# Optimization experiments

Measured on AMD Instinct MI355X. Metric: run time of the kernel, lower is better.

The kernel has to match this reference:

```python
import jax, jax.numpy as jnp
import numpy as np

D = 1024          # hidden_dim
S = 128           # seq_len
DECAY = 0.99
SPARSITY = 0.05
INHIB = 1.5       # inhibition_factor
TOPK = max(1, int(D * SPARSITY))  # = 51


def sparsify(x):
    """ReLU + keep top-k fraction (threshold = k-th largest of relu(x))."""
    pos = jax.nn.relu(x)
    thr = jax.lax.top_k(pos, TOPK)[0][-1]  # k-th largest value
    mask = (pos >= thr).astype(pos.dtype)
    return pos * mask


def setup_inputs() -> dict:
    key = jax.random.key(0)
    k1, k2 = jax.random.split(key)
    embeddings = jax.random.normal(k1, (S, D), dtype=jnp.float32)
    contradiction_scores = jax.random.uniform(k2, (S,), dtype=jnp.float32)
    return {"embeddings": embeddings, "contradiction_scores": contradiction_scores}


def reference(embeddings, contradiction_scores):
    """BDHScanner.process_sequence: sequential Hebbian updates with key=value=token.

    Returns (drift_scores [S], states [S, D, D]) — per-token drift and the
    state snapshot after each step, matching the torch module's outputs.
    """
    def step(state, inp):
        x, c = inp
        s = sparsify(x)                      # key == value vector (sparsified once)
        expectation = s @ state              # [D] GEVM against DxD state
        drift = jnp.linalg.norm(s - expectation)
        # excitatory - inhibitory = outer(k, v) * (1 - c * INHIB)
        update = jnp.outer(s, s) * (1.0 - c * INHIB)
        new_state = jax.nn.relu(state * DECAY + update)
        return new_state, (drift, new_state)

    state0 = jnp.zeros((D, D), dtype=jnp.float32)
    _, (drifts, states) = jax.lax.scan(step, state0, (embeddings, contradiction_scores))
    return drifts, states
```

## Files before the change

### kernel.cpp

```cpp
#include <hip/hip_runtime.h>

#define SEQ 128
#define DIM 1024
#define TOPK 51
#define DECAY 0.99f
#define INHIB 1.5f

__global__ __launch_bounds__(256) void sparsify_kernel(
    const float* __restrict__ emb, float* __restrict__ s_out,
    int* __restrict__ nnz_idx, int* __restrict__ nnz_cnt)
{
    const int t   = blockIdx.x;
    const int tid = threadIdx.x;
    const float* x = emb + t * DIM;

    float    v[4];
    unsigned u[4];
#pragma unroll
    for (int e = 0; e < 4; ++e) {
        float val = fmaxf(x[e * 256 + tid], 0.0f);
        v[e] = val;
        u[e] = __float_as_uint(val);
    }

    __shared__ unsigned hist[256];
    __shared__ unsigned sh_prefix;
    __shared__ unsigned sh_k;
    __shared__ int      sh_cnt;
    if (tid == 0) { sh_prefix = 0u; sh_k = TOPK; sh_cnt = 0; }
    __syncthreads();

    for (int pass = 0; pass < 4; ++pass) {
        const int shift = 24 - 8 * pass;
        const unsigned prefix = sh_prefix;
        hist[tid] = 0u;
        __syncthreads();
#pragma unroll
        for (int e = 0; e < 4; ++e) {
            bool ok;
            if (pass == 0) ok = true;
            else           ok = ((u[e] >> (shift + 8)) == (prefix >> (shift + 8)));
            if (ok) atomicAdd(&hist[(u[e] >> shift) & 255u], 1u);
        }
        __syncthreads();
        if (tid == 0) {
            unsigned k = sh_k, cum = 0;
            int b = 255;
            for (; b > 0; --b) { cum += hist[b]; if (cum >= k) break; }
            if (cum < k) { cum += hist[0]; }
            sh_k      = k - (cum - hist[b]);
            sh_prefix = prefix | ((unsigned)b << shift);
        }
        __syncthreads();
    }

    const float thr = __uint_as_float(sh_prefix);
#pragma unroll
    for (int e = 0; e < 4; ++e) {
        const int idx = e * 256 + tid;
        const float sval = (v[e] >= thr) ? v[e] : 0.0f;
        s_out[t * DIM + idx] = sval;
        if (sval > 0.0f) {
            int pos = atomicAdd(&sh_cnt, 1);
            nnz_idx[t * DIM + pos] = idx;
        }
    }
    __syncthreads();
    if (tid == 0) nnz_cnt[t] = sh_cnt;
}

__global__ __launch_bounds__(256) void evolve_kernel(
    const float* __restrict__ s, const float* __restrict__ con,
    float* __restrict__ states)
{
    const int i0 = blockIdx.x * 4;
    const int j0 = threadIdx.x * 4;

    float st[4][4];
#pragma unroll
    for (int a = 0; a < 4; ++a)
#pragma unroll
        for (int b = 0; b < 4; ++b) st[a][b] = 0.0f;

    for (int t = 0; t < SEQ; ++t) {
        const float f = 1.0f - INHIB * con[t];
        const float4 sj = *(const float4*)(s + t * DIM + j0);
        float si[4];
#pragma unroll
        for (int a = 0; a < 4; ++a) si[a] = s[t * DIM + i0 + a] * f;

        float* outp = states + (size_t)t * DIM * DIM;
#pragma unroll
        for (int a = 0; a < 4; ++a) {
            float4 o;
            o.x = fmaxf(0.0f, DECAY * st[a][0] + si[a] * sj.x);
            o.y = fmaxf(0.0f, DECAY * st[a][1] + si[a] * sj.y);
            o.z = fmaxf(0.0f, DECAY * st[a][2] + si[a] * sj.z);
            o.w = fmaxf(0.0f, DECAY * st[a][3] + si[a] * sj.w);
            st[a][0] = o.x; st[a][1] = o.y; st[a][2] = o.z; st[a][3] = o.w;
            *(float4*)(outp + (size_t)(i0 + a) * DIM + j0) = o;
        }
    }
}

__global__ __launch_bounds__(256) void drift_kernel(
    const float* __restrict__ s, const int* __restrict__ nnz_idx,
    const int* __restrict__ nnz_cnt, const float* __restrict__ states,
    float* __restrict__ drift)
{
    const int t   = blockIdx.x;
    const int tid = threadIdx.x;
    const int j0  = tid * 4;

    float e0 = 0.f, e1 = 0.f, e2 = 0.f, e3 = 0.f;
    if (t > 0) {
        const float* prev = states + (size_t)(t - 1) * DIM * DIM;
        const int cnt = nnz_cnt[t];
        for (int n = 0; n < cnt; ++n) {
            const int i = nnz_idx[t * DIM + n];
            const float si = s[t * DIM + i];
            const float4 row = *(const float4*)(prev + (size_t)i * DIM + j0);
            e0 += si * row.x; e1 += si * row.y;
            e2 += si * row.z; e3 += si * row.w;
        }
    }
    const float4 sj = *(const float4*)(s + t * DIM + j0);
    const float d0 = sj.x - e0, d1 = sj.y - e1, d2 = sj.z - e2, d3 = sj.w - e3;
    float local = d0 * d0 + d1 * d1 + d2 * d2 + d3 * d3;

#pragma unroll
    for (int off = 32; off > 0; off >>= 1)
        local += __shfl_down(local, off, 64);

    __shared__ float wsum[4];
    if ((tid & 63) == 0) wsum[tid >> 6] = local;
    __syncthreads();
    if (tid == 0) drift[t] = sqrtf(wsum[0] + wsum[1] + wsum[2] + wsum[3]);
}

extern "C" void kernel_launch(void* const* d_in, const int* in_sizes, int n_in,
                              void* d_out, int out_size, void* d_ws, size_t ws_size,
                              hipStream_t stream)
{
    const float* emb = (const float*)d_in[0];
    const float* con = (const float*)d_in[1];

    float* drift  = (float*)d_out;
    float* states = (float*)d_out + SEQ;

    float* s_buf   = (float*)d_ws;
    int*   nnz_idx = (int*)((char*)d_ws + (size_t)SEQ * DIM * 4);
    int*   nnz_cnt = (int*)((char*)d_ws + (size_t)2 * SEQ * DIM * 4);

    sparsify_kernel<<<SEQ, 256, 0, stream>>>(emb, s_buf, nnz_idx, nnz_cnt);
    evolve_kernel<<<DIM / 4, 256, 0, stream>>>(s_buf, con, states);
    drift_kernel<<<SEQ, 256, 0, stream>>>(s_buf, nnz_idx, nnz_cnt, states, drift);
}
```

Baseline: 616.1 us.

## Parallelize radix-select scan, widen evolve grid, split drift across four blocks

The top-k radix select now uses a wave-shuffle suffix scan over the histogram instead of a serial thread-0 loop. The evolve kernel gives each block one row instead of four, so it launches four times as many blocks. The drift kernel splits each token across four blocks, stages the nonzero indices and values in shared memory, and accumulates squared partial sums atomically. A small finish kernel then takes the square root. This is meant to raise occupancy and parallelism for the bandwidth-bound state writes and the drift reads, at the cost of an extra launch and atomics.

```diff
diff --git a/kernel.cpp b/kernel.cpp
--- a/kernel.cpp
+++ b/kernel.cpp
@@ -8,10 +8,13 @@
 
 __global__ __launch_bounds__(256) void sparsify_kernel(
     const float* __restrict__ emb, float* __restrict__ s_out,
-    int* __restrict__ nnz_idx, int* __restrict__ nnz_cnt)
+    int* __restrict__ nnz_idx, int* __restrict__ nnz_cnt,
+    float* __restrict__ drift2)
 {
-    const int t   = blockIdx.x;
-    const int tid = threadIdx.x;
+    const int t    = blockIdx.x;
+    const int tid  = threadIdx.x;
+    const int lane = tid & 63;
+    const int wave = tid >> 6;
     const float* x = emb + t * DIM;
 
     float    v[4];
@@ -24,17 +27,18 @@
     }
 
     __shared__ unsigned hist[256];
+    __shared__ unsigned wtot[4];
     __shared__ unsigned sh_prefix;
     __shared__ unsigned sh_k;
     __shared__ int      sh_cnt;
-    if (tid == 0) { sh_prefix = 0u; sh_k = TOPK; sh_cnt = 0; }
+    if (tid == 0) { sh_prefix = 0u; sh_k = TOPK; sh_cnt = 0; drift2[t] = 0.0f; }
+    hist[tid] = 0u;
     __syncthreads();
 
     for (int pass = 0; pass < 4; ++pass) {
         const int shift = 24 - 8 * pass;
         const unsigned prefix = sh_prefix;
-        hist[tid] = 0u;
-        __syncthreads();
+        const unsigned k      = sh_k;
 #pragma unroll
         for (int e = 0; e < 4; ++e) {
             bool ok;
@@ -43,14 +47,26 @@
             if (ok) atomicAdd(&hist[(u[e] >> shift) & 255u], 1u);
         }
         __syncthreads();
-        if (tid == 0) {
-            unsigned k = sh_k, cum = 0;
-            int b = 255;
-            for (; b > 0; --b) { cum += hist[b]; if (cum >= k) break; }
-            if (cum < k) { cum += hist[0]; }
-            sh_k      = k - (cum - hist[b]);
-            sh_prefix = prefix | ((unsigned)b << shift);
+
+        unsigned val = hist[tid];
+#pragma unroll
+        for (int off = 1; off < 64; off <<= 1) {
+            unsigned tmp = __shfl_down(val, off, 64);
+            if (lane + off < 64) val += tmp;
         }
+        if (lane == 0) wtot[wave] = val;
+        __syncthreads();
+
+        unsigned addHigher = 0u;
+        for (int w = wave + 1; w < 4; ++w) addHigher += wtot[w];
+        const unsigned scanFull = val + addHigher;
+        const unsigned nxtWithin = __shfl_down(scanFull, 1, 64);
+        const unsigned nxt = (lane == 63) ? addHigher : nxtWithin;
+        if (scanFull >= k && nxt < k) {
+            sh_prefix = prefix | ((unsigned)tid << shift);
+            sh_k      = k - nxt;
+        }
+        hist[tid] = 0u;
         __syncthreads();
     }
 
@@ -73,60 +89,56 @@
     const float* __restrict__ s, const float* __restrict__ con,
     float* __restrict__ states)
 {
-    const int i0 = blockIdx.x * 4;
+    const int i  = blockIdx.x;
     const int j0 = threadIdx.x * 4;
 
-    float st[4][4];
-#pragma unroll
-    for (int a = 0; a < 4; ++a)
-#pragma unroll
-        for (int b = 0; b < 4; ++b) st[a][b] = 0.0f;
+    float st[4] = {0.f, 0.f, 0.f, 0.f};
 
     for (int t = 0; t < SEQ; ++t) {
-        const float f = 1.0f - INHIB * con[t];
+        const float f  = 1.0f - INHIB * con[t];
         const float4 sj = *(const float4*)(s + t * DIM + j0);
-        float si[4];
-#pragma unroll
-        for (int a = 0; a < 4; ++a) si[a] = s[t * DIM + i0 + a] * f;
+        const float si = s[t * DIM + i] * f;
 
-        float* outp = states + (size_t)t * DIM * DIM;
-#pragma unroll
-        for (int a = 0; a < 4; ++a) {
-            float4 o;
-            o.x = fmaxf(0.0f, DECAY * st[a][0] + si[a] * sj.x);
-            o.y = fmaxf(0.0f, DECAY * st[a][1] + si[a] * sj.y);
-            o.z = fmaxf(0.0f, DECAY * st[a][2] + si[a] * sj.z);
-            o.w = fmaxf(0.0f, DECAY * st[a][3] + si[a] * sj.w);
-            st[a][0] = o.x; st[a][1] = o.y; st[a][2] = o.z; st[a][3] = o.w;
-            *(float4*)(outp + (size_t)(i0 + a) * DIM + j0) = o;
-        }
+        float4 o;
+        o.x = fmaxf(0.0f, DECAY * st[0] + si * sj.x);
+        o.y = fmaxf(0.0f, DECAY * st[1] + si * sj.y);
+        o.z = fmaxf(0.0f, DECAY * st[2] + si * sj.z);
+        o.w = fmaxf(0.0f, DECAY * st[3] + si * sj.w);
+        st[0] = o.x; st[1] = o.y; st[2] = o.z; st[3] = o.w;
+        *(float4*)(states + (size_t)t * DIM * DIM + (size_t)i * DIM + j0) = o;
     }
 }
 
 __global__ __launch_bounds__(256) void drift_kernel(
     const float* __restrict__ s, const int* __restrict__ nnz_idx,
     const int* __restrict__ nnz_cnt, const float* __restrict__ states,
-    float* __restrict__ drift)
+    float* __restrict__ drift2)
 {
-    const int t   = blockIdx.x;
+    const int t   = blockIdx.x >> 2;
+    const int q   = blockIdx.x & 3;
     const int tid = threadIdx.x;
-    const int j0  = tid * 4;
+    const int j   = q * 256 + tid;
 
-    float e0 = 0.f, e1 = 0.f, e2 = 0.f, e3 = 0.f;
+    __shared__ int   sh_ix[DIM];
+    __shared__ float sh_sv[DIM];
+
+    float e = 0.0f;
     if (t > 0) {
+        const int cnt = nnz_cnt[t];
+        for (int n = tid; n < cnt; n += 256) {
+            const int i = nnz_idx[t * DIM + n];
+            sh_ix[n] = i;
+            sh_sv[n] = s[t * DIM + i];
+        }
+        __syncthreads();
+
         const float* prev = states + (size_t)(t - 1) * DIM * DIM;
-        const int cnt = nnz_cnt[t];
-        for (int n = 0; n < cnt; ++n) {
-            const int i = nnz_idx[t * DIM + n];
-            const float si = s[t * DIM + i];
-            const float4 row = *(const float4*)(prev + (size_t)i * DIM + j0);
-            e0 += si * row.x; e1 += si * row.y;
-            e2 += si * row.z; e3 += si * row.w;
-        }
+#pragma unroll 4
+        for (int n = 0; n < cnt; ++n)
+            e += sh_sv[n] * prev[(size_t)sh_ix[n] * DIM + j];
     }
-    const float4 sj = *(const float4*)(s + t * DIM + j0);
-    const float d0 = sj.x - e0, d1 = sj.y - e1, d2 = sj.z - e2, d3 = sj.w - e3;
-    float local = d0 * d0 + d1 * d1 + d2 * d2 + d3 * d3;
+    const float d = s[t * DIM + j] - e;
+    float local = d * d;
 
 #pragma unroll
     for (int off = 32; off > 0; off >>= 1)
@@ -135,7 +147,15 @@
     __shared__ float wsum[4];
     if ((tid & 63) == 0) wsum[tid >> 6] = local;
     __syncthreads();
-    if (tid == 0) drift[t] = sqrtf(wsum[0] + wsum[1] + wsum[2] + wsum[3]);
+    if (tid == 0)
+        atomicAdd(&drift2[t], wsum[0] + wsum[1] + wsum[2] + wsum[3]);
+}
+
+__global__ void finish_kernel(const float* __restrict__ drift2,
+                              float* __restrict__ drift)
+{
+    const int t = threadIdx.x;
+    if (t < SEQ) drift[t] = sqrtf(drift2[t]);
 }
 
 extern "C" void kernel_launch(void* const* d_in, const int* in_sizes, int n_in,
@@ -151,8 +171,10 @@
     float* s_buf   = (float*)d_ws;
     int*   nnz_idx = (int*)((char*)d_ws + (size_t)SEQ * DIM * 4);
     int*   nnz_cnt = (int*)((char*)d_ws + (size_t)2 * SEQ * DIM * 4);
+    float* drift2  = (float*)((char*)d_ws + (size_t)2 * SEQ * DIM * 4 + SEQ * 4);
 
-    sparsify_kernel<<<SEQ, 256, 0, stream>>>(emb, s_buf, nnz_idx, nnz_cnt);
-    evolve_kernel<<<DIM / 4, 256, 0, stream>>>(s_buf, con, states);
-    drift_kernel<<<SEQ, 256, 0, stream>>>(s_buf, nnz_idx, nnz_cnt, states, drift);
+    sparsify_kernel<<<SEQ, 256, 0, stream>>>(emb, s_buf, nnz_idx, nnz_cnt, drift2);
+    evolve_kernel<<<DIM, 256, 0, stream>>>(s_buf, con, states);
+    drift_kernel<<<SEQ * 4, 256, 0, stream>>>(s_buf, nnz_idx, nnz_cnt, states, drift2);
+    finish_kernel<<<1, 128, 0, stream>>>(drift2, drift);
 }
```

After: 556.0 us. -9.7%, faster.
